# Optimization experiments

Hardware: AMD Instinct MI355X
Metric: run time of the kernel (lower is better)

Reference implementation:

```python
import jax, jax.numpy as jnp
import numpy as np

N_EMBD = 2048
QKV_EMBD = 2048
N_HEAD = 32
N_KV_HEAD = 8
HEAD_DIM = QKV_EMBD // N_HEAD  # 64
GROUPS = N_HEAD // N_KV_HEAD   # 4
ROPE_THETA = 10000.0
SCALE = float(np.sqrt(HEAD_DIM))


def setup_inputs() -> dict:
    key = jax.random.key(0)
    ks = jax.random.split(key, 12)
    B, S = 2, 2048
    inp = {
        "query": jax.random.normal(ks[0], (B, S, N_EMBD), jnp.float32),
        "key": jax.random.normal(ks[1], (B, S, N_EMBD), jnp.float32),
        "value": jax.random.normal(ks[2], (B, S, N_EMBD), jnp.float32),
        "mask": jnp.ones((B, S), dtype=bool),
        "Wq": jax.random.normal(ks[3], (QKV_EMBD, N_EMBD), jnp.float32) * 0.02,
        "bq": jnp.zeros((QKV_EMBD,), jnp.float32),
        "Wk": jax.random.normal(ks[4], (N_KV_HEAD * HEAD_DIM, N_EMBD), jnp.float32) * 0.02,
        "bk": jnp.zeros((N_KV_HEAD * HEAD_DIM,), jnp.float32),
        "Wv": jax.random.normal(ks[5], (N_KV_HEAD * HEAD_DIM, N_EMBD), jnp.float32) * 0.02,
        "bv": jnp.zeros((N_KV_HEAD * HEAD_DIM,), jnp.float32),
        "Wo": jax.random.normal(ks[6], (N_EMBD, QKV_EMBD), jnp.float32) * 0.02,
        "bo": jnp.zeros((N_EMBD,), jnp.float32),
    }
    return inp


def _rotate_half(x):
    d = x.shape[-1] // 2
    return jnp.concatenate([-x[..., d:], x[..., :d]], axis=-1)


def _rope_cos_sin(seq_len, dtype):
    # rope_factor == 1.0 -> no NTK adjustment; is_causal -> position_ids = arange
    inv_freq = 1.0 / (ROPE_THETA ** (jnp.arange(0, HEAD_DIM, 2, dtype=jnp.float32) / HEAD_DIM))
    pos = jnp.arange(seq_len, dtype=jnp.float32)
    freqs = jnp.einsum("i,j->ij", pos, inv_freq)           # [S, D/2]
    emb = jnp.concatenate([freqs, freqs], axis=-1)          # [S, D]
    return jnp.cos(emb).astype(dtype)[None, None], jnp.sin(emb).astype(dtype)[None, None]


def reference(query, key, value, mask, Wq, bq, Wk, bk, Wv, bv, Wo, bo):
    B, S, _ = query.shape
    Q = (query @ Wq.T + bq).reshape(B, S, N_HEAD, HEAD_DIM).transpose(0, 2, 1, 3)      # [B,H,S,D]
    K = (key @ Wk.T + bk).reshape(B, S, N_KV_HEAD, HEAD_DIM).transpose(0, 2, 1, 3)     # [B,KV,S,D]
    V = (value @ Wv.T + bv).reshape(B, S, N_KV_HEAD, HEAD_DIM).transpose(0, 2, 1, 3)

    cos, sin = _rope_cos_sin(S, Q.dtype)
    Q = Q * cos + _rotate_half(Q) * sin
    K = K * cos + _rotate_half(K) * sin

    # interleaved GQA repeat: each kv head serves GROUPS consecutive query heads
    K = jnp.repeat(K, GROUPS, axis=1)  # [B,H,S,D]
    V = jnp.repeat(V, GROUPS, axis=1)

    attn = jnp.einsum("bhqd,bhkd->bhqk", Q, K)              # [B,H,S,S]
    causal = jnp.tril(jnp.ones((S, S), dtype=bool))
    full_mask = mask[:, None, None, :] & causal[None, None]  # [B,1,S,S]
    attn = jnp.where(full_mask, attn, jnp.finfo(attn.dtype).min)
    attn_weights = jax.nn.softmax(attn / SCALE, axis=-1)     # dropout p=0 (eval)
    out = jnp.einsum("bhqk,bhkd->bhqd", attn_weights, V)
    out = out.transpose(0, 2, 1, 3).reshape(B, S, QKV_EMBD)
    return out @ Wo.T + bo
```

## Files before the change

### kernel.cpp

```cpp
#include <hip/hip_runtime.h>
#include <hip/hip_bf16.h>
#include <cmath>

#define NE   2048
#define NH   32
#define NKV  8
#define HD   64
#define SEQ  2048
#define NB   2

typedef __attribute__((ext_vector_type(4))) float f32x4;
typedef __attribute__((ext_vector_type(16))) float f32x16;
typedef __attribute__((ext_vector_type(8))) short bf16x8;
typedef __attribute__((ext_vector_type(4))) short bf16x4;

typedef const __attribute__((address_space(1))) void cgvoid;
typedef __attribute__((address_space(3))) void lvoid;

#define QSCALE 0.18033688011112042f

__device__ __forceinline__ short f2bf(float f) {
  union { float f; unsigned u; } v; v.f = f;
  unsigned r = v.u + 0x7fffu + ((v.u >> 16) & 1u);
  return (short)(r >> 16);
}

__device__ __forceinline__ unsigned cvt_pk_bf16(float a, float b) {
  unsigned r;
  asm("v_cvt_pk_bf16_f32 %0, %1, %2" : "=v"(r) : "v"(a), "v"(b));
  return r;
}

__global__ __launch_bounds__(256) void cvt_all(
    const float* __restrict__ s0, short* __restrict__ d0,
    const float* __restrict__ s1, short* __restrict__ d1,
    const float* __restrict__ s2, short* __restrict__ d2,
    const float* __restrict__ s3, short* __restrict__ d3,
    const float* __restrict__ s4, short* __restrict__ d4,
    const float* __restrict__ s5, short* __restrict__ d5,
    const float* __restrict__ s6, short* __restrict__ d6)
{
  int idx = blockIdx.x * 256 + threadIdx.x;
  const float* s; short* d; int rel;
  if      (idx < 1048576) { s = s0; d = d0; rel = idx; }
  else if (idx < 2097152) { s = s1; d = d1; rel = idx - 1048576; }
  else if (idx < 3145728) { s = s2; d = d2; rel = idx - 2097152; }
  else if (idx < 3670016) { s = s3; d = d3; rel = idx - 3145728; }
  else if (idx < 3801088) { s = s4; d = d4; rel = idx - 3670016; }
  else if (idx < 3932160) { s = s5; d = d5; rel = idx - 3801088; }
  else                    { s = s6; d = d6; rel = idx - 3932160; }
  size_t off = (size_t)rel * 8;
  f32x4 a = *(const f32x4*)(s + off);
  f32x4 b = *(const f32x4*)(s + off + 4);
  bf16x8 o;
  #pragma unroll
  for (int j = 0; j < 4; ++j) { o[j] = f2bf(a[j]); o[4 + j] = f2bf(b[j]); }
  *(bf16x8*)(d + off) = o;
}

template<int EPI>
__device__ __forceinline__ void gemm256_body(
    short* As, short* Ws, int m0, int n0,
    const short* __restrict__ A, const short* __restrict__ W,
    const float* __restrict__ bias, void* __restrict__ Cout, int K)
{
  const int t = threadIdx.x, lane = t & 63, w = t >> 6;
  const int lr = lane & 15, lg = lane >> 4;
  const int wm = (w >> 2) * 128, wn = (w & 3) * 64;

  f32x4 acc[8][4];
  #pragma unroll
  for (int i = 0; i < 8; ++i)
    #pragma unroll
    for (int j = 0; j < 4; ++j) acc[i][j] = (f32x4){0.f, 0.f, 0.f, 0.f};

  auto STAGE = [&](int kt) {
    const int k0 = kt << 6;
    short* Ad = As + (kt & 1) * 16384;
    short* Wd = Ws + (kt & 1) * 16384;
    #pragma unroll
    for (int it = 0; it < 4; ++it) {
      int e = it * 512 + t, r = e >> 3, c = e & 7;
      int cs = ((c ^ (r & 7)) << 3);
      __builtin_amdgcn_global_load_lds((cgvoid*)(A + (size_t)(m0 + r) * K + k0 + cs),
                                       (lvoid*)(Ad + e * 8), 16, 0, 0);
      __builtin_amdgcn_global_load_lds((cgvoid*)(W + (size_t)(n0 + r) * K + k0 + cs),
                                       (lvoid*)(Wd + e * 8), 16, 0, 0);
    }
  };

  const int nt = K >> 6;
  STAGE(0);

  for (int ti = 0; ti < nt; ++ti) {
    const short* Ab = As + (ti & 1) * 16384;
    const short* Wb = Ws + (ti & 1) * 16384;
    if (ti + 1 < nt) {
      STAGE(ti + 1);
      asm volatile("s_waitcnt vmcnt(8)" ::: "memory");
    } else {
      asm volatile("s_waitcnt vmcnt(0)" ::: "memory");
    }
    __builtin_amdgcn_s_barrier();

    bf16x8 wf[2][4];
    #pragma unroll
    for (int ks = 0; ks < 2; ++ks)
      #pragma unroll
      for (int nf = 0; nf < 4; ++nf) {
        int row = wn + nf * 16 + lr;
        wf[ks][nf] = *(const bf16x8*)(Wb + row * 64 + (((ks * 4 + lg) ^ (row & 7)) << 3));
      }
    #pragma unroll
    for (int mq = 0; mq < 4; ++mq) {
      bf16x8 af[2][2];
      #pragma unroll
      for (int ks = 0; ks < 2; ++ks)
        #pragma unroll
        for (int mi = 0; mi < 2; ++mi) {
          int row = wm + (mq * 2 + mi) * 16 + lr;
          af[ks][mi] = *(const bf16x8*)(Ab + row * 64 + (((ks * 4 + lg) ^ (row & 7)) << 3));
        }
      __builtin_amdgcn_s_setprio(1);
      #pragma unroll
      for (int ks = 0; ks < 2; ++ks)
        #pragma unroll
        for (int mi = 0; mi < 2; ++mi)
          #pragma unroll
          for (int nf = 0; nf < 4; ++nf)
            acc[mq * 2 + mi][nf] =
                __builtin_amdgcn_mfma_f32_16x16x32_bf16(af[ks][mi], wf[ks][nf],
                                                        acc[mq * 2 + mi][nf], 0, 0, 0);
      __builtin_amdgcn_s_setprio(0);
    }
    __builtin_amdgcn_s_barrier();
  }

  if (EPI == 1) {
    short* C = (short*)Cout;
    #pragma unroll
    for (int mf = 0; mf < 8; ++mf)
      #pragma unroll
      for (int nf = 0; nf < 4; ++nf) {
        int n = n0 + wn + nf * 16 + lr;
        int kv = n >> 6, d = n & 63;
        int mb = m0 + wm + mf * 16 + lg * 4;
        int b = mb >> 11, s = mb & (SEQ - 1);
        bf16x4 pb;
        #pragma unroll
        for (int i = 0; i < 4; ++i) pb[i] = f2bf(acc[mf][nf][i] + bias[n]);
        *(bf16x4*)(C + (((size_t)b * NKV + kv) * HD + d) * SEQ + s) = pb;
      }
  } else {
    const int HN = (EPI == 2) ? NH : NKV;
    short* C = (short*)Cout;
    #pragma unroll
    for (int mf = 0; mf < 8; ++mf)
      #pragma unroll
      for (int nf2 = 0; nf2 < 2; ++nf2) {
        int n1 = n0 + wn + nf2 * 16 + lr;
        int d1 = n1 & 63;
        int h = n1 >> 6;
        float inv = exp2f(-(float)d1 * (13.287712379549449f / 32.0f));
        #pragma unroll
        for (int i = 0; i < 4; ++i) {
          int m = m0 + wm + mf * 16 + lg * 4 + i;
          int b = m >> 11, s = m & (SEQ - 1);
          float v1 = acc[mf][nf2][i] + bias[n1];
          float v2 = acc[mf][nf2 + 2][i] + bias[n1 + 32];
          float ang = (float)s * inv;
          float c, sn;
          __sincosf(ang, &sn, &c);
          float o1 = v1 * c - v2 * sn;
          float o2 = v2 * c + v1 * sn;
          if (EPI == 2) { o1 *= QSCALE; o2 *= QSCALE; }
          size_t base = (((size_t)b * HN + h) * SEQ + s) * HD;
          C[base + d1]      = f2bf(o1);
          C[base + d1 + 32] = f2bf(o2);
        }
      }
  }
}

__global__ __launch_bounds__(512, 2) void gemm_qkv256(
    const short* __restrict__ qA, const short* __restrict__ Wq,
    const float* __restrict__ bq, short* __restrict__ Qout,
    const short* __restrict__ kA, const short* __restrict__ Wk,
    const float* __restrict__ bk, short* __restrict__ Kout,
    const short* __restrict__ vA, const short* __restrict__ Wv,
    const float* __restrict__ bv, short* __restrict__ Vout)
{
  __shared__ __align__(16) short As[2 * 256 * 64];
  __shared__ __align__(16) short Ws[2 * 256 * 64];
  int orig = blockIdx.x;
  int bid = (orig & 7) * 24 + (orig >> 3);
  if (bid < 128) {
    gemm256_body<2>(As, Ws, (bid & 15) * 256, (bid >> 4) * 256, qA, Wq, bq, (void*)Qout, NE);
  } else if (bid < 160) {
    int b2 = bid - 128;
    gemm256_body<3>(As, Ws, (b2 & 15) * 256, (b2 >> 4) * 256, kA, Wk, bk, (void*)Kout, NE);
  } else {
    int b2 = bid - 160;
    gemm256_body<1>(As, Ws, (b2 & 15) * 256, (b2 >> 4) * 256, vA, Wv, bv, (void*)Vout, NE);
  }
}

__global__ __launch_bounds__(256) void gemm_o(
    const short* __restrict__ A, const short* __restrict__ W,
    const float* __restrict__ bias, float* __restrict__ C, int N, int K)
{
  __shared__ __align__(16) short As[2 * 128 * 64];
  __shared__ __align__(16) short Ws[2 * 128 * 64];
  const int t = threadIdx.x, lane = t & 63, w = t >> 6;
  const int lr = lane & 15, lg = lane >> 4;
  const int wm = (w >> 1) * 64, wn = (w & 1) * 64;
  const int L = blockIdx.x;
  const int xcd = L & 7, slot = L >> 3;
  const int bx = xcd + 8 * (slot >> 4);
  const int byy = slot & 15;
  const int m0 = bx * 128, n0 = byy * 128;

  f32x4 acc[4][4];
  #pragma unroll
  for (int i = 0; i < 4; ++i)
    #pragma unroll
    for (int j = 0; j < 4; ++j) acc[i][j] = (f32x4){0.f, 0.f, 0.f, 0.f};

  const int nt = K >> 6;
  #pragma unroll
  for (int it = 0; it < 4; ++it) {
    int e = it * 256 + t, r = e >> 3, c = e & 7;
    int cs = ((c ^ (r & 7)) << 3);
    __builtin_amdgcn_global_load_lds((cgvoid*)(A + (size_t)(m0 + r) * K + cs),
                                     (lvoid*)(As + e * 8), 16, 0, 0);
    __builtin_amdgcn_global_load_lds((cgvoid*)(W + (size_t)(n0 + r) * K + cs),
                                     (lvoid*)(Ws + e * 8), 16, 0, 0);
  }

  for (int ti = 0; ti < nt; ++ti) {
    const int cur = ti & 1;
    const short* Ab = As + cur * 8192;
    const short* Wb = Ws + cur * 8192;
    if (ti + 1 < nt) {
      const int k0 = (ti + 1) << 6;
      short* An = As + (cur ^ 1) * 8192;
      short* Wn = Ws + (cur ^ 1) * 8192;
      #pragma unroll
      for (int it = 0; it < 4; ++it) {
        int e = it * 256 + t, r = e >> 3, c = e & 7;
        int cs = ((c ^ (r & 7)) << 3);
        __builtin_amdgcn_global_load_lds((cgvoid*)(A + (size_t)(m0 + r) * K + k0 + cs),
                                         (lvoid*)(An + e * 8), 16, 0, 0);
        __builtin_amdgcn_global_load_lds((cgvoid*)(W + (size_t)(n0 + r) * K + k0 + cs),
                                         (lvoid*)(Wn + e * 8), 16, 0, 0);
      }
      asm volatile("s_waitcnt vmcnt(8)" ::: "memory");
    } else {
      asm volatile("s_waitcnt vmcnt(0)" ::: "memory");
    }
    __builtin_amdgcn_s_barrier();
    __builtin_amdgcn_sched_barrier(0);

    bf16x8 wf[2][4];
    #pragma unroll
    for (int ks = 0; ks < 2; ++ks)
      #pragma unroll
      for (int nf = 0; nf < 4; ++nf) {
        int row = wn + nf * 16 + lr;
        wf[ks][nf] = *(const bf16x8*)(Wb + row * 64 + (((ks * 4 + lg) ^ (row & 7)) << 3));
      }
    #pragma unroll
    for (int mq = 0; mq < 2; ++mq) {
      bf16x8 af[2][2];
      #pragma unroll
      for (int ks = 0; ks < 2; ++ks)
        #pragma unroll
        for (int mi = 0; mi < 2; ++mi) {
          int row = wm + (mq * 2 + mi) * 16 + lr;
          af[ks][mi] = *(const bf16x8*)(Ab + row * 64 + (((ks * 4 + lg) ^ (row & 7)) << 3));
        }
      __builtin_amdgcn_s_setprio(1);
      #pragma unroll
      for (int ks = 0; ks < 2; ++ks)
        #pragma unroll
        for (int mi = 0; mi < 2; ++mi)
          #pragma unroll
          for (int nf = 0; nf < 4; ++nf)
            acc[mq * 2 + mi][nf] =
                __builtin_amdgcn_mfma_f32_16x16x32_bf16(af[ks][mi], wf[ks][nf],
                                                        acc[mq * 2 + mi][nf], 0, 0, 0);
      __builtin_amdgcn_s_setprio(0);
      __builtin_amdgcn_s_barrier();
      __builtin_amdgcn_sched_barrier(0);
    }
  }

  #pragma unroll
  for (int mf = 0; mf < 4; ++mf)
    #pragma unroll
    for (int nf = 0; nf < 4; ++nf)
      #pragma unroll
      for (int i = 0; i < 4; ++i) {
        int m = m0 + wm + mf * 16 + lg * 4 + i;
        int n = n0 + wn + nf * 16 + lr;
        C[(size_t)m * N + n] = acc[mf][nf][i] + bias[n];
      }
}

__global__ __launch_bounds__(256) void attn_kernel(
    const short* __restrict__ Q, const short* __restrict__ K,
    const short* __restrict__ Vt, short* __restrict__ O)
{
  __shared__ __align__(16) short Ks[2][64 * 64];
  __shared__ __align__(16) short Vs[2][64 * 64];

  const int t = threadIdx.x, lane = t & 63, w = t >> 6;
  const int l31 = lane & 31, hi = lane >> 5;
  const int L = blockIdx.x;
  const int xcd = L & 7, slot = L >> 3;
  const int by = xcd + 8 * (slot >> 5);
  const int bx = slot & 31;
  const int b = by >> 3, kvh = by & 7;
  const int h = kvh * 4 + w;

  const short* Qh = Q + ((size_t)b * NH + h) * SEQ * HD;
  const short* Kh = K + ((size_t)b * NKV + kvh) * SEQ * HD;
  const short* Vh = Vt + ((size_t)b * NKV + kvh) * (size_t)HD * SEQ;

  #pragma unroll 1
  for (int pass = 0; pass < 2; ++pass) {
    const int qb32 = pass ? bx : (63 - bx);
    const int q0 = qb32 * 32;
    const int ntile = (qb32 >> 1) + 1;
    const int qpos = q0 + l31;

    bf16x8 qfr[4];
    #pragma unroll
    for (int dd = 0; dd < 4; ++dd)
      qfr[dd] = *(const bf16x8*)(Qh + (size_t)(q0 + l31) * HD + dd * 16 + hi * 8);

    f32x16 o[2];
    #pragma unroll
    for (int dh = 0; dh < 2; ++dh)
      #pragma unroll
      for (int r = 0; r < 16; ++r) o[dh][r] = 0.f;
    float lsum = 0.f;

    #pragma unroll
    for (int it = 0; it < 2; ++it) {
      int cid = it * 256 + t;
      int r = cid >> 3, c = cid & 7;
      int cs = ((c ^ (r & 7)) << 3);
      __builtin_amdgcn_global_load_lds((cgvoid*)(Kh + (size_t)r * HD + cs),
                                       (lvoid*)(Ks[0] + cid * 8), 16, 0, 0);
      __builtin_amdgcn_global_load_lds((cgvoid*)(Vh + (size_t)r * SEQ + cs),
                                       (lvoid*)(Vs[0] + cid * 8), 16, 0, 0);
    }
    __syncthreads();

    for (int ti = 0; ti < ntile; ++ti) {
      const int cur = ti & 1;
      if (ti + 1 < ntile) {
        const int kvn = (ti + 1) * 64;
        #pragma unroll
        for (int it = 0; it < 2; ++it) {
          int cid = it * 256 + t;
          int r = cid >> 3, c = cid & 7;
          int cs = ((c ^ (r & 7)) << 3);
          __builtin_amdgcn_global_load_lds((cgvoid*)(Kh + (size_t)(kvn + r) * HD + cs),
                                           (lvoid*)(Ks[cur ^ 1] + cid * 8), 16, 0, 0);
          __builtin_amdgcn_global_load_lds((cgvoid*)(Vh + (size_t)r * SEQ + kvn + cs),
                                           (lvoid*)(Vs[cur ^ 1] + cid * 8), 16, 0, 0);
        }
      }
      const int kv0 = ti * 64;
      const short* Kb = Ks[cur];
      const short* Vb = Vs[cur];

      f32x16 p[2];
      __builtin_amdgcn_s_setprio(1);
      #pragma unroll
      for (int f = 0; f < 2; ++f) {
        f32x16 z;
        #pragma unroll
        for (int r = 0; r < 16; ++r) z[r] = 0.f;
        #pragma unroll
        for (int dd = 0; dd < 4; ++dd) {
          int row = f * 32 + l31;
          bf16x8 ka = *(const bf16x8*)(Kb + row * 64 + (((2 * dd + hi) ^ (row & 7)) << 3));
          z = __builtin_amdgcn_mfma_f32_32x32x16_bf16(ka, qfr[dd], z, 0, 0, 0);
        }
        p[f] = z;
      }
      __builtin_amdgcn_s_setprio(0);

      if (ti == ntile - 1) {
        #pragma unroll
        for (int f = 0; f < 2; ++f)
          #pragma unroll
          for (int r = 0; r < 16; ++r) {
            int kpos = kv0 + f * 32 + (r & 3) + 8 * (r >> 2) + 4 * hi;
            if (kpos > qpos) p[f][r] = -INFINITY;
          }
      }

      unsigned pa[4][4];
      #pragma unroll
      for (int f = 0; f < 2; ++f) {
        float e[16];
        #pragma unroll
        for (int r = 0; r < 16; ++r) {
          e[r] = __builtin_amdgcn_exp2f(p[f][r]);
          lsum += e[r];
        }
        unsigned c[8];
        #pragma unroll
        for (int i = 0; i < 8; ++i) c[i] = cvt_pk_bf16(e[2 * i], e[2 * i + 1]);
        asm volatile("v_permlane32_swap_b32 %0, %1" : "+v"(c[0]), "+v"(c[2]));
        asm volatile("v_permlane32_swap_b32 %0, %1" : "+v"(c[1]), "+v"(c[3]));
        asm volatile("v_permlane32_swap_b32 %0, %1" : "+v"(c[4]), "+v"(c[6]));
        asm volatile("v_permlane32_swap_b32 %0, %1" : "+v"(c[5]), "+v"(c[7]));
        pa[2 * f][0] = c[0]; pa[2 * f][1] = c[1]; pa[2 * f][2] = c[2]; pa[2 * f][3] = c[3];
        pa[2 * f + 1][0] = c[4]; pa[2 * f + 1][1] = c[5];
        pa[2 * f + 1][2] = c[6]; pa[2 * f + 1][3] = c[7];
      }

      __builtin_amdgcn_s_setprio(1);
      #pragma unroll
      for (int ks = 0; ks < 4; ++ks) {
        bf16x8 paf = *(const bf16x8*)&pa[ks][0];
        #pragma unroll
        for (int dh = 0; dh < 2; ++dh) {
          int row = dh * 32 + l31;
          bf16x8 vb = *(const bf16x8*)(Vb + row * 64 + (((2 * ks + hi) ^ (row & 7)) << 3));
          o[dh] = __builtin_amdgcn_mfma_f32_32x32x16_bf16(paf, vb, o[dh], 0, 0, 0);
        }
      }
      __builtin_amdgcn_s_setprio(0);
      __syncthreads();
    }

    lsum += __shfl_xor(lsum, 32);
    #pragma unroll
    for (int r = 0; r < 16; ++r) {
      int crow = (r & 3) + 8 * (r >> 2) + 4 * hi;
      float li = __shfl(lsum, crow, 64);
      float invl = 1.0f / li;
      int s = q0 + crow;
      size_t base = (((size_t)b * SEQ + s) * NH + h) * HD;
      O[base + l31]      = f2bf(o[0][r] * invl);
      O[base + 32 + l31] = f2bf(o[1][r] * invl);
    }
  }
}

extern "C" void kernel_launch(void* const* d_in, const int* in_sizes, int n_in,
                              void* d_out, int out_size, void* d_ws, size_t ws_size,
                              hipStream_t stream) {
  (void)in_sizes; (void)n_in; (void)out_size; (void)ws_size;
  const float* q  = (const float*)d_in[0];
  const float* k  = (const float*)d_in[1];
  const float* v  = (const float*)d_in[2];
  const float* Wq = (const float*)d_in[4];
  const float* bq = (const float*)d_in[5];
  const float* Wk = (const float*)d_in[6];
  const float* bk = (const float*)d_in[7];
  const float* Wv = (const float*)d_in[8];
  const float* bv = (const float*)d_in[9];
  const float* Wo = (const float*)d_in[10];
  const float* bo = (const float*)d_in[11];

  const size_t SQ2 = (size_t)NB * SEQ * NE;
  const size_t W1  = (size_t)NE * NE;
  const size_t W2  = (size_t)(NKV * HD) * NE;
  const size_t KVN = (size_t)NB * NKV * SEQ * HD;

  short* ws = (short*)d_ws;
  short* qb  = ws;
  short* kb  = ws + SQ2;
  short* vb  = ws + 2 * SQ2;
  short* Wqb = ws + 3 * SQ2;
  short* Wkb = Wqb + W1;
  short* Wvb = Wkb + W2;
  short* Wob = Wvb + W2;
  short* Qr  = Wob + W1;
  short* Kr  = Qr + SQ2;
  short* Vr  = Kr + KVN;
  short* Ob  = qb;

  dim3 blk(256);

  cvt_all<<<17408, blk, 0, stream>>>(q, qb, k, kb, v, vb, Wq, Wqb, Wk, Wkb, Wv, Wvb, Wo, Wob);
  gemm_qkv256<<<192, dim3(512), 0, stream>>>(qb, Wqb, bq, Qr, kb, Wkb, bk, Kr, vb, Wvb, bv, Vr);
  attn_kernel<<<512, blk, 0, stream>>>(Qr, Kr, Vr, Ob);
  gemm_o<<<512, blk, 0, stream>>>(Ob, Wob, bo, (float*)d_out, NE, NE);
}
```

Measured before the change: 195.8 us.

## Fuse fp32-to-bf16 activation conversion into QKV GEMM A-tile loading

Removes the separate bf16 conversion pass over the query/key/value activations. The QKV GEMM now loads fp32 A tiles into registers, converts them with packed bf16 instructions, and writes them to LDS, while the weights still go through direct global-to-LDS loads. The change avoids writing and re-reading about 48 MB of intermediate bf16 activations. In exchange the GEMM moves twice the A bytes per tile through registers, adding register pressure and LDS write work inside the main loop.

```diff
diff --git a/kernel.cpp b/kernel.cpp
--- a/kernel.cpp
+++ b/kernel.cpp
@@ -13,6 +13,7 @@
 typedef __attribute__((ext_vector_type(16))) float f32x16;
 typedef __attribute__((ext_vector_type(8))) short bf16x8;
 typedef __attribute__((ext_vector_type(4))) short bf16x4;
+typedef __attribute__((ext_vector_type(4))) unsigned u32x4;
 
 typedef const __attribute__((address_space(1))) void cgvoid;
 typedef __attribute__((address_space(3))) void lvoid;
@@ -31,24 +32,18 @@
   return r;
 }
 
-__global__ __launch_bounds__(256) void cvt_all(
+__global__ __launch_bounds__(256) void cvt_w(
     const float* __restrict__ s0, short* __restrict__ d0,
     const float* __restrict__ s1, short* __restrict__ d1,
     const float* __restrict__ s2, short* __restrict__ d2,
-    const float* __restrict__ s3, short* __restrict__ d3,
-    const float* __restrict__ s4, short* __restrict__ d4,
-    const float* __restrict__ s5, short* __restrict__ d5,
-    const float* __restrict__ s6, short* __restrict__ d6)
+    const float* __restrict__ s3, short* __restrict__ d3)
 {
   int idx = blockIdx.x * 256 + threadIdx.x;
   const float* s; short* d; int rel;
-  if      (idx < 1048576) { s = s0; d = d0; rel = idx; }
-  else if (idx < 2097152) { s = s1; d = d1; rel = idx - 1048576; }
-  else if (idx < 3145728) { s = s2; d = d2; rel = idx - 2097152; }
-  else if (idx < 3670016) { s = s3; d = d3; rel = idx - 3145728; }
-  else if (idx < 3801088) { s = s4; d = d4; rel = idx - 3670016; }
-  else if (idx < 3932160) { s = s5; d = d5; rel = idx - 3801088; }
-  else                    { s = s6; d = d6; rel = idx - 3932160; }
+  if      (idx < 524288)  { s = s0; d = d0; rel = idx; }
+  else if (idx < 655360)  { s = s1; d = d1; rel = idx - 524288; }
+  else if (idx < 786432)  { s = s2; d = d2; rel = idx - 655360; }
+  else                    { s = s3; d = d3; rel = idx - 786432; }
   size_t off = (size_t)rel * 8;
   f32x4 a = *(const f32x4*)(s + off);
   f32x4 b = *(const f32x4*)(s + off + 4);
@@ -61,7 +56,7 @@
 template<int EPI>
 __device__ __forceinline__ void gemm256_body(
     short* As, short* Ws, int m0, int n0,
-    const short* __restrict__ A, const short* __restrict__ W,
+    const float* __restrict__ A, const short* __restrict__ W,
     const float* __restrict__ bias, void* __restrict__ Cout, int K)
 {
   const int t = threadIdx.x, lane = t & 63, w = t >> 6;
@@ -74,30 +69,58 @@
     #pragma unroll
     for (int j = 0; j < 4; ++j) acc[i][j] = (f32x4){0.f, 0.f, 0.f, 0.f};
 
-  auto STAGE = [&](int kt) {
+  auto STAGE_W = [&](int kt) {
     const int k0 = kt << 6;
-    short* Ad = As + (kt & 1) * 16384;
     short* Wd = Ws + (kt & 1) * 16384;
     #pragma unroll
     for (int it = 0; it < 4; ++it) {
       int e = it * 512 + t, r = e >> 3, c = e & 7;
       int cs = ((c ^ (r & 7)) << 3);
-      __builtin_amdgcn_global_load_lds((cgvoid*)(A + (size_t)(m0 + r) * K + k0 + cs),
-                                       (lvoid*)(Ad + e * 8), 16, 0, 0);
       __builtin_amdgcn_global_load_lds((cgvoid*)(W + (size_t)(n0 + r) * K + k0 + cs),
                                        (lvoid*)(Wd + e * 8), 16, 0, 0);
     }
   };
 
+  f32x4 areg[4][2];
+  auto LOAD_A = [&](int kt) {
+    const int k0 = kt << 6;
+    #pragma unroll
+    for (int it = 0; it < 4; ++it) {
+      int e = it * 512 + t, r = e >> 3, c = e & 7;
+      int cs = ((c ^ (r & 7)) << 3);
+      const float* src = A + (size_t)(m0 + r) * K + k0 + cs;
+      areg[it][0] = *(const f32x4*)(src);
+      areg[it][1] = *(const f32x4*)(src + 4);
+    }
+  };
+  auto WRITE_A = [&](int kt) {
+    short* Ad = As + (kt & 1) * 16384;
+    #pragma unroll
+    for (int it = 0; it < 4; ++it) {
+      int e = it * 512 + t;
+      u32x4 v;
+      v[0] = cvt_pk_bf16(areg[it][0][0], areg[it][0][1]);
+      v[1] = cvt_pk_bf16(areg[it][0][2], areg[it][0][3]);
+      v[2] = cvt_pk_bf16(areg[it][1][0], areg[it][1][1]);
+      v[3] = cvt_pk_bf16(areg[it][1][2], areg[it][1][3]);
+      *(u32x4*)(Ad + e * 8) = v;
+    }
+  };
+
   const int nt = K >> 6;
-  STAGE(0);
+
+  STAGE_W(0);
+  LOAD_A(0);
+  WRITE_A(0);
+  asm volatile("s_waitcnt lgkmcnt(0)" ::: "memory");
 
   for (int ti = 0; ti < nt; ++ti) {
     const short* Ab = As + (ti & 1) * 16384;
     const short* Wb = Ws + (ti & 1) * 16384;
     if (ti + 1 < nt) {
-      STAGE(ti + 1);
-      asm volatile("s_waitcnt vmcnt(8)" ::: "memory");
+      STAGE_W(ti + 1);
+      LOAD_A(ti + 1);
+      asm volatile("s_waitcnt vmcnt(12)" ::: "memory");
     } else {
       asm volatile("s_waitcnt vmcnt(0)" ::: "memory");
     }
@@ -133,6 +156,8 @@
                                                         acc[mq * 2 + mi][nf], 0, 0, 0);
       __builtin_amdgcn_s_setprio(0);
     }
+    if (ti + 1 < nt) WRITE_A(ti + 1);
+    asm volatile("s_waitcnt lgkmcnt(0)" ::: "memory");
     __builtin_amdgcn_s_barrier();
   }
 
@@ -183,11 +208,11 @@
 }
 
 __global__ __launch_bounds__(512, 2) void gemm_qkv256(
-    const short* __restrict__ qA, const short* __restrict__ Wq,
+    const float* __restrict__ qA, const short* __restrict__ Wq,
     const float* __restrict__ bq, short* __restrict__ Qout,
-    const short* __restrict__ kA, const short* __restrict__ Wk,
+    const float* __restrict__ kA, const short* __restrict__ Wk,
     const float* __restrict__ bk, short* __restrict__ Kout,
-    const short* __restrict__ vA, const short* __restrict__ Wv,
+    const float* __restrict__ vA, const short* __restrict__ Wv,
     const float* __restrict__ bv, short* __restrict__ Vout)
 {
   __shared__ __align__(16) short As[2 * 256 * 64];
@@ -476,22 +501,19 @@
   const size_t KVN = (size_t)NB * NKV * SEQ * HD;
 
   short* ws = (short*)d_ws;
-  short* qb  = ws;
-  short* kb  = ws + SQ2;
-  short* vb  = ws + 2 * SQ2;
-  short* Wqb = ws + 3 * SQ2;
+  short* Wqb = ws;
   short* Wkb = Wqb + W1;
   short* Wvb = Wkb + W2;
   short* Wob = Wvb + W2;
   short* Qr  = Wob + W1;
   short* Kr  = Qr + SQ2;
   short* Vr  = Kr + KVN;
-  short* Ob  = qb;
+  short* Ob  = Vr + KVN;
 
   dim3 blk(256);
 
-  cvt_all<<<17408, blk, 0, stream>>>(q, qb, k, kb, v, vb, Wq, Wqb, Wk, Wkb, Wv, Wvb, Wo, Wob);
-  gemm_qkv256<<<192, dim3(512), 0, stream>>>(qb, Wqb, bq, Qr, kb, Wkb, bk, Kr, vb, Wvb, bv, Vr);
+  cvt_w<<<5120, blk, 0, stream>>>(Wq, Wqb, Wk, Wkb, Wv, Wvb, Wo, Wob);
+  gemm_qkv256<<<192, dim3(512), 0, stream>>>(q, Wqb, bq, Qr, k, Wkb, bk, Kr, v, Wvb, bv, Vr);
   attn_kernel<<<512, blk, 0, stream>>>(Qr, Kr, Vr, Ob);
   gemm_o<<<512, blk, 0, stream>>>(Ob, Wob, bo, (float*)d_out, NE, NE);
 }
```

New measurement: 192.6 us. Within noise of the previous version (-1.6%).
